# Kernel optimization log

Hardware: AMD Instinct MI355X
Metric: run time of the kernel (lower is better)

Reference implementation:

```python
import jax, jax.numpy as jnp
import numpy as np

HIDDEN = 2560
NUM_HEADS = 32
HEAD_DIM = HIDDEN // NUM_HEADS          # 80
ROTARY_DIM = int(0.4 * HEAD_DIM)        # 32 (partial rotary)
ROPE_BASE = 10000.0
SCALE = HEAD_DIM ** -0.5


def _apply_partial_rope(x, pos):
    # x: [B, S, H, D], pos: [B, S] int. NeoX-style rotation on first ROTARY_DIM dims.
    half = ROTARY_DIM // 2
    inv_freq = 1.0 / (ROPE_BASE ** (jnp.arange(half, dtype=jnp.float32) / half))
    ang = pos.astype(jnp.float32)[..., None] * inv_freq      # [B, S, half]
    cos = jnp.cos(ang)[:, :, None, :]                        # [B, S, 1, half]
    sin = jnp.sin(ang)[:, :, None, :]
    x1 = x[..., :half]
    x2 = x[..., half:ROTARY_DIM]
    x_pass = x[..., ROTARY_DIM:]
    o1 = x1 * cos - x2 * sin
    o2 = x2 * cos + x1 * sin
    return jnp.concatenate([o1, o2, x_pass], axis=-1)


def setup_inputs() -> dict:
    key = jax.random.key(0)
    ks = jax.random.split(key, 5)
    B, S = 2, 2048
    hidden_states = jax.random.normal(ks[0], (B, S, HIDDEN), dtype=jnp.float32)
    position_ids = jnp.tile(jnp.arange(S, dtype=jnp.int32)[None, :], (B, 1))
    w_std = HIDDEN ** -0.5
    Wqkv = jax.random.normal(ks[1], (HIDDEN, 3 * HIDDEN), dtype=jnp.float32) * w_std
    bqkv = jax.random.normal(ks[2], (3 * HIDDEN,), dtype=jnp.float32) * 0.02
    Wd = jax.random.normal(ks[3], (HIDDEN, HIDDEN), dtype=jnp.float32) * w_std
    bd = jax.random.normal(ks[4], (HIDDEN,), dtype=jnp.float32) * 0.02
    return {"position_ids": position_ids, "hidden_states": hidden_states,
            "Wqkv": Wqkv, "bqkv": bqkv, "Wd": Wd, "bd": bd}


def reference(position_ids, hidden_states, Wqkv, bqkv, Wd, bd):
    B, S, _ = hidden_states.shape
    qkv = hidden_states @ Wqkv + bqkv                         # [B, S, 3*HIDDEN]
    q, k, v = jnp.split(qkv, 3, axis=-1)
    q = q.reshape(B, S, NUM_HEADS, HEAD_DIM)
    k = k.reshape(B, S, NUM_HEADS, HEAD_DIM)
    v = v.reshape(B, S, NUM_HEADS, HEAD_DIM)
    q = _apply_partial_rope(q, position_ids)
    k = _apply_partial_rope(k, position_ids)
    # causal self-attention (RadixAttention prefill with empty prefix)
    scores = jnp.einsum('bqhd,bkhd->bhqk', q, k) * SCALE      # [B, H, S, S]
    causal = jnp.tril(jnp.ones((S, S), dtype=bool))
    scores = jnp.where(causal[None, None], scores, jnp.finfo(scores.dtype).min)
    probs = jax.nn.softmax(scores, axis=-1)
    attn = jnp.einsum('bhqk,bkhd->bqhd', probs, v).reshape(B, S, HIDDEN)
    return attn @ Wd + bd
```

## Files before the change

### kernel.cpp

```cpp
#include <hip/hip_runtime.h>

#define HIDDEN 2560
#define NHEADS 32
#define HDIM 80
#define DPAD 96
#define SEQ 2048
#define M_TOK 4096
#define N_QKV 7680
#define ATT_SCALE 0.11180339887498949f

typedef __attribute__((ext_vector_type(4))) float f32x4;
typedef __attribute__((ext_vector_type(16))) float f32x16;
typedef __attribute__((ext_vector_type(4))) int i32x4;
typedef __attribute__((ext_vector_type(8))) short bf16x8;
typedef __attribute__((ext_vector_type(8))) unsigned short ushort8;

#define BAR() asm volatile("s_barrier" ::: "memory")

__device__ __forceinline__ unsigned short f2bf(float f) {
    unsigned int u = __float_as_uint(f);
    u += 0x7FFFu + ((u >> 16) & 1u);
    return (unsigned short)(u >> 16);
}
__device__ __forceinline__ float bf2f(unsigned short h) {
    return __uint_as_float(((unsigned int)h) << 16);
}

__device__ __forceinline__ void async_copy16(unsigned short* lds, const unsigned short* g) {
    __builtin_amdgcn_global_load_lds((const __attribute__((address_space(1))) void*)g,
                                     (__attribute__((address_space(3))) void*)lds, 16, 0, 0);
}

__device__ __forceinline__ int cvt_pk_bf16(float lo, float hi) {
    int d;
    asm("v_cvt_pk_bf16_f32 %0, %1, %2" : "=v"(d) : "v"(lo), "v"(hi));
    return d;
}

__global__ __launch_bounds__(256) void cvt_kernel(const float* __restrict__ in,
                                                  unsigned short* __restrict__ out, int n8) {
    int i = blockIdx.x * 256 + threadIdx.x;
    if (i >= n8) return;
    const float4* p = (const float4*)in + (size_t)i * 2;
    float4 a = p[0], b = p[1];
    ushort8 o;
    o[0] = f2bf(a.x); o[1] = f2bf(a.y); o[2] = f2bf(a.z); o[3] = f2bf(a.w);
    o[4] = f2bf(b.x); o[5] = f2bf(b.y); o[6] = f2bf(b.z); o[7] = f2bf(b.w);
    *((ushort8*)out + i) = o;
}

__global__ __launch_bounds__(256) void transpose_kernel(const float* __restrict__ in,
                                                        unsigned short* __restrict__ out,
                                                        int R, int C) {
    __shared__ unsigned short tile[64][66];
    const int r0 = blockIdx.y * 64, c0 = blockIdx.x * 64;
    const int t = threadIdx.x;
#pragma unroll
    for (int rep = 0; rep < 16; ++rep) {
        int idx = rep * 256 + t;
        int i = idx >> 6, j = idx & 63;
        tile[i][j] = f2bf(in[(size_t)(r0 + i) * C + (c0 + j)]);
    }
    __syncthreads();
#pragma unroll
    for (int rep = 0; rep < 16; ++rep) {
        int idx = rep * 256 + t;
        int j = idx >> 6, i = idx & 63;
        out[(size_t)(c0 + j) * R + (r0 + i)] = tile[i][j];
    }
}

template <int OUT_BF16>
__global__ __launch_bounds__(512, 2) void gemm256(const unsigned short* __restrict__ A,
                                                  const unsigned short* __restrict__ Bt,
                                                  const float* __restrict__ bias,
                                                  void* __restrict__ C,
                                                  int M, int N, int K) {
    __shared__ __align__(16) unsigned short S[4][16384];
    const int t = threadIdx.x;
    const int lane = t & 63, wid = t >> 6;
    const int wm = wid >> 2, wn = wid & 3;
    const int l15 = lane & 15, lhi = lane >> 4;

    const int cpx = (int)gridDim.x >> 3;
    const int wg = ((int)blockIdx.x % 8) * cpx + ((int)blockIdx.x >> 3);
    const int bm = (wg & 15) * 256;
    const int bn = (wg >> 4) * 256;

    int srow[2], scol[2];
#pragma unroll
    for (int c = 0; c < 2; ++c) {
        int idx = t + c * 512;
        srow[c] = idx >> 2;
        scol[c] = ((idx & 3) ^ ((srow[c] >> 1) & 3)) * 8;
    }
    const unsigned short* Abase = A + (size_t)bm * K;
    const unsigned short* Bbase = Bt + (size_t)bn * K;
    const int NT = K >> 6;

    int aoff[8], boff[4];
#pragma unroll
    for (int i = 0; i < 8; ++i) {
        int r = wm * 128 + i * 16 + l15;
        aoff[i] = r * 32 + ((lhi ^ ((r >> 1) & 3)) * 8);
    }
#pragma unroll
    for (int f = 0; f < 4; ++f) {
        int r = wn * 64 + f * 16 + l15;
        boff[f] = 8192 + r * 32 + ((lhi ^ ((r >> 1) & 3)) * 8);
    }

    f32x4 acc[8][4] = {};

#define STAGE_A(J) { const int j_ = (J); unsigned short* d = &S[j_ & 3][0];            \
    _Pragma("unroll")                                                                  \
    for (int c = 0; c < 2; ++c)                                                        \
        async_copy16(d + (t + c * 512) * 8,                                            \
                     Abase + (size_t)srow[c] * K + j_ * 32 + scol[c]); }
#define STAGE_B(J) { const int j_ = (J); unsigned short* d = &S[j_ & 3][8192];         \
    _Pragma("unroll")                                                                  \
    for (int c = 0; c < 2; ++c)                                                        \
        async_copy16(d + (t + c * 512) * 8,                                            \
                     Bbase + (size_t)srow[c] * K + j_ * 32 + scol[c]); }

#define PERIOD(J, VM, DOSTAGE) {                                                       \
    const int jp_ = (J);                                                               \
    asm volatile("s_waitcnt vmcnt(" #VM ")" ::: "memory");                             \
    BAR();                                                                             \
    const unsigned short* sl = &S[jp_ & 3][0];                                         \
    if (DOSTAGE) STAGE_A(jp_ + 3);                                                     \
    bf16x8 bq[4], afr[4];                                                              \
    _Pragma("unroll")                                                                  \
    for (int f = 0; f < 4; ++f) bq[f] = *(const bf16x8*)(sl + boff[f]);                \
    _Pragma("unroll")                                                                  \
    for (int i = 0; i < 4; ++i) afr[i] = *(const bf16x8*)(sl + aoff[i]);               \
    __builtin_amdgcn_s_setprio(1);                                                     \
    _Pragma("unroll")                                                                  \
    for (int i = 0; i < 4; ++i)                                                        \
        _Pragma("unroll")                                                              \
        for (int f = 0; f < 4; ++f)                                                    \
            acc[i][f] = __builtin_amdgcn_mfma_f32_16x16x32_bf16(afr[i], bq[f],         \
                                                                acc[i][f], 0, 0, 0);   \
    __builtin_amdgcn_s_setprio(0);                                                     \
    if (DOSTAGE) STAGE_B(jp_ + 3);                                                     \
    _Pragma("unroll")                                                                  \
    for (int i = 0; i < 4; ++i) afr[i] = *(const bf16x8*)(sl + aoff[4 + i]);           \
    __builtin_amdgcn_s_setprio(1);                                                     \
    _Pragma("unroll")                                                                  \
    for (int i = 0; i < 4; ++i)                                                        \
        _Pragma("unroll")                                                              \
        for (int f = 0; f < 4; ++f)                                                    \
            acc[4 + i][f] = __builtin_amdgcn_mfma_f32_16x16x32_bf16(afr[i], bq[f],     \
                                                                    acc[4 + i][f],     \
                                                                    0, 0, 0);          \
    __builtin_amdgcn_s_setprio(0); }

    STAGE_A(0); STAGE_B(0);
    STAGE_A(1); STAGE_B(1);
    STAGE_A(2); STAGE_B(2);

    for (int T = 0; T < NT - 2; ++T) {
        PERIOD(2 * T, 8, 1);
        PERIOD(2 * T + 1, 8, 1);
    }
    PERIOD(2 * NT - 4, 8, 1);
    PERIOD(2 * NT - 3, 8, 0);
    PERIOD(2 * NT - 2, 4, 0);
    PERIOD(2 * NT - 1, 0, 0);

#undef PERIOD
#undef STAGE_A
#undef STAGE_B

#pragma unroll
    for (int f = 0; f < 4; ++f) {
        const int col = bn + wn * 64 + f * 16 + l15;
        const float bv = bias[col];
#pragma unroll
        for (int i = 0; i < 8; ++i) {
            const int row0 = bm + wm * 128 + i * 16 + lhi * 4;
#pragma unroll
            for (int r = 0; r < 4; ++r) {
                float v = acc[i][f][r] + bv;
                if (OUT_BF16)
                    ((unsigned short*)C)[(size_t)(row0 + r) * N + col] = f2bf(v);
                else
                    ((float*)C)[(size_t)(row0 + r) * N + col] = v;
            }
        }
    }
}

__global__ __launch_bounds__(256) void pack_rope_kernel(const unsigned short* __restrict__ qkv,
                                                        const int* __restrict__ pos_ids,
                                                        unsigned short* __restrict__ Qb,
                                                        unsigned short* __restrict__ Kb,
                                                        unsigned short* __restrict__ Vt) {
    int g = blockIdx.x * 256 + threadIdx.x;
    int s = g & (SEQ - 1);
    int bh = g >> 11;
    int b = bh >> 5;
    int h = bh & 31;
    int m = b * SEQ + s;
    const unsigned short* base = qkv + (size_t)m * N_QKV + h * HDIM;
    unsigned short* Qrow = Qb + ((size_t)bh * SEQ + s) * DPAD;
    unsigned short* Krow = Kb + ((size_t)bh * SEQ + s) * DPAD;
    unsigned short* Vcol = Vt + (size_t)bh * HDIM * SEQ + s;

    float pos = (float)pos_ids[m];
    float qv[32], kv[32];
#pragma unroll
    for (int c = 0; c < 4; ++c) {
        ushort8 qc = *(const ushort8*)(base + c * 8);
        ushort8 kc = *(const ushort8*)(base + HIDDEN + c * 8);
#pragma unroll
        for (int j = 0; j < 8; ++j) {
            qv[c * 8 + j] = bf2f(qc[j]);
            kv[c * 8 + j] = bf2f(kc[j]);
        }
    }
#pragma unroll
    for (int d = 0; d < 16; ++d) {
        float inv = __expf(-(float)d * 0.5756462732485115f);
        float ang = pos * inv;
        float sn, cs;
        __sincosf(ang, &sn, &cs);
        float qcs = cs * ATT_SCALE, qsn = sn * ATT_SCALE;
        float x1 = qv[d], x2 = qv[d + 16];
        qv[d] = x1 * qcs - x2 * qsn;
        qv[d + 16] = x2 * qcs + x1 * qsn;
        x1 = kv[d]; x2 = kv[d + 16];
        kv[d] = x1 * cs - x2 * sn;
        kv[d + 16] = x2 * cs + x1 * sn;
    }
#pragma unroll
    for (int c = 0; c < 4; ++c) {
        ushort8 qo, ko;
#pragma unroll
        for (int j = 0; j < 8; ++j) {
            qo[j] = f2bf(qv[c * 8 + j]);
            ko[j] = f2bf(kv[c * 8 + j]);
        }
        *(ushort8*)(Qrow + c * 8) = qo;
        *(ushort8*)(Krow + c * 8) = ko;
    }
#pragma unroll
    for (int c = 4; c < 10; ++c) {
        ushort8 qc = *(const ushort8*)(base + c * 8);
        ushort8 qo;
#pragma unroll
        for (int j = 0; j < 8; ++j) qo[j] = f2bf(bf2f(qc[j]) * ATT_SCALE);
        *(ushort8*)(Qrow + c * 8) = qo;
        *(ushort8*)(Krow + c * 8) = *(const ushort8*)(base + HIDDEN + c * 8);
    }
#pragma unroll
    for (int d = 0; d < HDIM; ++d) Vcol[(size_t)d * SEQ] = base[2 * HIDDEN + d];
}

__global__ __launch_bounds__(512) void flash_kernel(const unsigned short* __restrict__ Qb,
                                                    const unsigned short* __restrict__ Kb,
                                                    const unsigned short* __restrict__ Vt,
                                                    unsigned short* __restrict__ attn) {
    __shared__ __align__(16) unsigned short Klds[64 * 128];
    __shared__ __align__(16) unsigned short Vlds[96 * 64];

    const int bh = blockIdx.x;
    const int qb = 7 - (int)blockIdx.y;
    const int q0b = qb * 256;
    const int nkt = 4 * qb + 4;
    const int t = threadIdx.x;
    const int lane = t & 63, wid = t >> 6;
    const int l31 = lane & 31, h = lane >> 5, l7 = lane & 7;
    const int q0w = q0b + wid * 32;
    const int swz = l7 << 3;

    const unsigned short* Kbase = Kb + (size_t)bh * SEQ * DPAD;
    const unsigned short* Vbase = Vt + (size_t)bh * HDIM * SEQ;

    bf16x8 qf[5];
    {
        const unsigned short* Qrow = Qb + ((size_t)bh * SEQ + q0w + l31) * DPAD + h * 8;
#pragma unroll
        for (int dc = 0; dc < 5; ++dc) qf[dc] = *(const bf16x8*)(Qrow + dc * 16);
    }

    ((int*)Vlds)[2560 + t] = 0;

    f32x16 acc0 = {}, acc1 = {}, acc2 = {};
    float mrow = -1e30f, lrow = 0.f;

    const int kidx1 = 512 + t;
    const int kr0 = t / 10, kc0 = t % 10;
    const int kr1 = kidx1 / 10, kc1 = kidx1 % 10;
    const int vr0 = t >> 3, vc0 = t & 7;
    const int vr1 = (512 + t) >> 3, vc1 = t & 7;
    const int kd0 = kr0 * 128 + ((kc0 * 8) ^ ((kr0 & 7) << 3));
    const int kd1 = kr1 * 128 + ((kc1 * 8) ^ ((kr1 & 7) << 3));
    const int vd0 = vr0 * 64 + ((vc0 * 8) ^ ((vr0 & 7) << 3));
    const int vd1 = vr1 * 64 + ((vc1 * 8) ^ ((vr1 & 7) << 3));

    ushort8 kreg0, kreg1, vreg0, vreg1;
    kreg0 = *(const ushort8*)(Kbase + (size_t)kr0 * DPAD + kc0 * 8);
    if (t < 128) kreg1 = *(const ushort8*)(Kbase + (size_t)kr1 * DPAD + kc1 * 8);
    vreg0 = *(const ushort8*)(Vbase + (size_t)vr0 * SEQ + vc0 * 8);
    if (t < 128) vreg1 = *(const ushort8*)(Vbase + (size_t)vr1 * SEQ + vc1 * 8);

    for (int kt = 0; kt < nkt; ++kt) {
        const int k0 = kt * 64;
        __syncthreads();
        *(ushort8*)(Klds + kd0) = kreg0;
        if (t < 128) *(ushort8*)(Klds + kd1) = kreg1;
        *(ushort8*)(Vlds + vd0) = vreg0;
        if (t < 128) *(ushort8*)(Vlds + vd1) = vreg1;
        __syncthreads();
        if (kt + 1 < nkt) {
            const int kn = k0 + 64;
            kreg0 = *(const ushort8*)(Kbase + (size_t)(kn + kr0) * DPAD + kc0 * 8);
            if (t < 128) kreg1 = *(const ushort8*)(Kbase + (size_t)(kn + kr1) * DPAD + kc1 * 8);
            vreg0 = *(const ushort8*)(Vbase + (size_t)vr0 * SEQ + kn + vc0 * 8);
            if (t < 128) vreg1 = *(const ushort8*)(Vbase + (size_t)vr1 * SEQ + kn + vc1 * 8);
        }
        if (k0 > q0w + 31) continue;

        f32x16 s0 = {}, s1 = {};
        __builtin_amdgcn_s_setprio(1);
#pragma unroll
        for (int dc = 0; dc < 5; ++dc) {
            const int co = (dc * 16 + h * 8) ^ swz;
            bf16x8 ka = *(const bf16x8*)(Klds + l31 * 128 + co);
            bf16x8 kb2 = *(const bf16x8*)(Klds + (32 + l31) * 128 + co);
            s0 = __builtin_amdgcn_mfma_f32_32x32x16_bf16(ka, qf[dc], s0, 0, 0, 0);
            s1 = __builtin_amdgcn_mfma_f32_32x32x16_bf16(kb2, qf[dc], s1, 0, 0, 0);
        }
        __builtin_amdgcn_s_setprio(0);

        const int qg = q0w + l31;
        if (k0 + 63 > q0w) {
#pragma unroll
            for (int r = 0; r < 16; ++r) {
                const int kg = k0 + (r & 3) + 8 * (r >> 2) + 4 * h;
                if (kg > qg) s0[r] = -2e30f;
                if (kg + 32 > qg) s1[r] = -2e30f;
            }
        }
        float pmax = s0[0];
#pragma unroll
        for (int r = 1; r < 16; ++r) pmax = fmaxf(pmax, s0[r]);
#pragma unroll
        for (int r = 0; r < 16; ++r) pmax = fmaxf(pmax, s1[r]);
        pmax = fmaxf(pmax, __shfl_xor(pmax, 32, 64));
        if (!__all(pmax <= mrow + 8.0f)) {
            float mnew = fmaxf(mrow, pmax);
            float scl = __expf(mrow - mnew);
            mrow = mnew;
            lrow *= scl;
#pragma unroll
            for (int r = 0; r < 16; ++r) {
                float sq = __shfl(scl, (r & 3) + 8 * (r >> 2) + 4 * h, 64);
                acc0[r] *= sq; acc1[r] *= sq; acc2[r] *= sq;
            }
        }
        float ps = 0.f;
#pragma unroll
        for (int r = 0; r < 16; ++r) { s0[r] = __expf(s0[r] - mrow); ps += s0[r]; }
#pragma unroll
        for (int r = 0; r < 16; ++r) { s1[r] = __expf(s1[r] - mrow); ps += s1[r]; }
        lrow += ps + __shfl_xor(ps, 32, 64);
        i32x4 af[2][2];
#pragma unroll
        for (int ks = 0; ks < 2; ++ks) {
            const f32x16& sv = ks ? s1 : s0;
            int pk0[2], pk1[2], pk2[2], pk3[2];
#pragma unroll
            for (int i = 0; i < 2; ++i) {
                pk0[i] = cvt_pk_bf16(sv[2 * i], sv[2 * i + 1]);
                pk1[i] = cvt_pk_bf16(sv[4 + 2 * i], sv[5 + 2 * i]);
                pk2[i] = cvt_pk_bf16(sv[8 + 2 * i], sv[9 + 2 * i]);
                pk3[i] = cvt_pk_bf16(sv[12 + 2 * i], sv[13 + 2 * i]);
            }
#pragma unroll
            for (int i = 0; i < 2; ++i) {
                const int o0 = __shfl_xor(pk0[i], 32, 64);
                const int o1 = __shfl_xor(pk1[i], 32, 64);
                af[ks][0][i]     = h ? o1     : pk0[i];
                af[ks][0][2 + i] = h ? pk1[i] : o0;
                const int o2 = __shfl_xor(pk2[i], 32, 64);
                const int o3 = __shfl_xor(pk3[i], 32, 64);
                af[ks][1][i]     = h ? o3     : pk2[i];
                af[ks][1][2 + i] = h ? pk3[i] : o2;
            }
        }
        __builtin_amdgcn_s_setprio(1);
#pragma unroll
        for (int ds = 0; ds < 3; ++ds) {
            f32x16& ac = ds == 0 ? acc0 : (ds == 1 ? acc1 : acc2);
            const int vrow = (ds * 32 + l31) * 64;
#pragma unroll
            for (int ks = 0; ks < 2; ++ks)
#pragma unroll
                for (int kh = 0; kh < 2; ++kh) {
                    bf16x8 vb = *(const bf16x8*)(Vlds + vrow + ((ks * 32 + kh * 16 + h * 8) ^ swz));
                    bf16x8 pa = __builtin_bit_cast(bf16x8, af[ks][kh]);
                    ac = __builtin_amdgcn_mfma_f32_32x32x16_bf16(pa, vb, ac, 0, 0, 0);
                }
        }
        __builtin_amdgcn_s_setprio(0);
    }

    const int hh = bh & 31, b = bh >> 5;
    const float linv = 1.0f / lrow;
#pragma unroll
    for (int r = 0; r < 16; ++r) {
        const int ql = (r & 3) + 8 * (r >> 2) + 4 * h;
        const float lv = __shfl(linv, ql, 64);
        const int row = b * SEQ + q0b + wid * 32 + ql;
        unsigned short* orow = attn + (size_t)row * HIDDEN + hh * HDIM;
        orow[l31] = f2bf(acc0[r] * lv);
        orow[32 + l31] = f2bf(acc1[r] * lv);
        if (l31 < 16) orow[64 + l31] = f2bf(acc2[r] * lv);
    }
}

extern "C" void kernel_launch(void* const* d_in, const int* in_sizes, int n_in,
                              void* d_out, int out_size, void* d_ws, size_t ws_size,
                              hipStream_t stream) {
    const int* pos = (const int*)d_in[0];
    const float* hid = (const float*)d_in[1];
    const float* Wqkv = (const float*)d_in[2];
    const float* bqkv = (const float*)d_in[3];
    const float* Wd = (const float*)d_in[4];
    const float* bd = (const float*)d_in[5];
    float* out = (float*)d_out;
    char* ws = (char*)d_ws;

    unsigned short* WqkvT = (unsigned short*)(ws);
    unsigned short* WdT   = (unsigned short*)(ws + 39321600);
    unsigned short* Xbf   = (unsigned short*)(ws + 52428800);
    unsigned short* qkv   = (unsigned short*)(ws + 73400320);
    unsigned short* Qbuf  = (unsigned short*)(ws + 136314880);
    unsigned short* Kbuf  = (unsigned short*)(ws + 161480704);
    unsigned short* Vt    = (unsigned short*)(ws + 186646528);
    unsigned short* attnb = Xbf;

    cvt_kernel<<<(M_TOK * HIDDEN / 8 + 255) / 256, 256, 0, stream>>>(hid, Xbf, M_TOK * HIDDEN / 8);
    transpose_kernel<<<dim3(N_QKV / 64, HIDDEN / 64), 256, 0, stream>>>(Wqkv, WqkvT, HIDDEN, N_QKV);
    transpose_kernel<<<dim3(HIDDEN / 64, HIDDEN / 64), 256, 0, stream>>>(Wd, WdT, HIDDEN, HIDDEN);
    gemm256<1><<<(M_TOK / 256) * (N_QKV / 256), 512, 0, stream>>>(Xbf, WqkvT, bqkv, qkv,
                                                                  M_TOK, N_QKV, HIDDEN);
    pack_rope_kernel<<<(64 * SEQ) / 256, 256, 0, stream>>>(qkv, pos, Qbuf, Kbuf, Vt);
    flash_kernel<<<dim3(64, 8), 512, 0, stream>>>(Qbuf, Kbuf, Vt, attnb);
    gemm256<0><<<(M_TOK / 256) * (HIDDEN / 256), 512, 0, stream>>>(attnb, WdT, bd, out,
                                                                   M_TOK, HIDDEN, HIDDEN);
}
```

Measured before the change: 387.8 us.

## Switch GEMM to double-buffered 64-wide K tiles with wider swizzle

```diff
diff --git a/kernel.cpp b/kernel.cpp
--- a/kernel.cpp
+++ b/kernel.cpp
@@ -76,7 +76,7 @@
                                                   const float* __restrict__ bias,
                                                   void* __restrict__ C,
                                                   int M, int N, int K) {
-    __shared__ __align__(16) unsigned short S[4][16384];
+    __shared__ __align__(16) unsigned short S[2][32768];
     const int t = threadIdx.x;
     const int lane = t & 63, wid = t >> 6;
     const int wm = wid >> 2, wn = wid & 3;
@@ -87,12 +87,12 @@
     const int bm = (wg & 15) * 256;
     const int bn = (wg >> 4) * 256;
 
-    int srow[2], scol[2];
-#pragma unroll
-    for (int c = 0; c < 2; ++c) {
+    int srow[4], scol[4];
+#pragma unroll
+    for (int c = 0; c < 4; ++c) {
         int idx = t + c * 512;
-        srow[c] = idx >> 2;
-        scol[c] = ((idx & 3) ^ ((srow[c] >> 1) & 3)) * 8;
+        srow[c] = idx >> 3;
+        scol[c] = ((idx & 7) ^ (srow[c] & 7)) * 8;
     }
     const unsigned short* Abase = A + (size_t)bm * K;
     const unsigned short* Bbase = Bt + (size_t)bn * K;
@@ -102,73 +102,75 @@
 #pragma unroll
     for (int i = 0; i < 8; ++i) {
         int r = wm * 128 + i * 16 + l15;
-        aoff[i] = r * 32 + ((lhi ^ ((r >> 1) & 3)) * 8);
+        aoff[i] = r * 64 + ((lhi ^ (r & 7)) * 8);
     }
 #pragma unroll
     for (int f = 0; f < 4; ++f) {
         int r = wn * 64 + f * 16 + l15;
-        boff[f] = 8192 + r * 32 + ((lhi ^ ((r >> 1) & 3)) * 8);
+        boff[f] = 16384 + r * 64 + ((lhi ^ (r & 7)) * 8);
     }
 
     f32x4 acc[8][4] = {};
 
-#define STAGE_A(J) { const int j_ = (J); unsigned short* d = &S[j_ & 3][0];            \
+#define STAGE_A(T1) { unsigned short* d = &S[(T1) & 1][0];                             \
     _Pragma("unroll")                                                                  \
-    for (int c = 0; c < 2; ++c)                                                        \
+    for (int c = 0; c < 4; ++c)                                                        \
         async_copy16(d + (t + c * 512) * 8,                                            \
-                     Abase + (size_t)srow[c] * K + j_ * 32 + scol[c]); }
-#define STAGE_B(J) { const int j_ = (J); unsigned short* d = &S[j_ & 3][8192];         \
+                     Abase + (size_t)srow[c] * K + (T1) * 64 + scol[c]); }
+#define STAGE_B(T1) { unsigned short* d = &S[(T1) & 1][16384];                         \
     _Pragma("unroll")                                                                  \
-    for (int c = 0; c < 2; ++c)                                                        \
+    for (int c = 0; c < 4; ++c)                                                        \
         async_copy16(d + (t + c * 512) * 8,                                            \
-                     Bbase + (size_t)srow[c] * K + j_ * 32 + scol[c]); }
-
-#define PERIOD(J, VM, DOSTAGE) {                                                       \
-    const int jp_ = (J);                                                               \
-    asm volatile("s_waitcnt vmcnt(" #VM ")" ::: "memory");                             \
-    BAR();                                                                             \
-    const unsigned short* sl = &S[jp_ & 3][0];                                         \
-    if (DOSTAGE) STAGE_A(jp_ + 3);                                                     \
-    bf16x8 bq[4], afr[4];                                                              \
-    _Pragma("unroll")                                                                  \
-    for (int f = 0; f < 4; ++f) bq[f] = *(const bf16x8*)(sl + boff[f]);                \
-    _Pragma("unroll")                                                                  \
-    for (int i = 0; i < 4; ++i) afr[i] = *(const bf16x8*)(sl + aoff[i]);               \
-    __builtin_amdgcn_s_setprio(1);                                                     \
-    _Pragma("unroll")                                                                  \
-    for (int i = 0; i < 4; ++i)                                                        \
-        _Pragma("unroll")                                                              \
-        for (int f = 0; f < 4; ++f)                                                    \
-            acc[i][f] = __builtin_amdgcn_mfma_f32_16x16x32_bf16(afr[i], bq[f],         \
-                                                                acc[i][f], 0, 0, 0);   \
-    __builtin_amdgcn_s_setprio(0);                                                     \
-    if (DOSTAGE) STAGE_B(jp_ + 3);                                                     \
-    _Pragma("unroll")                                                                  \
-    for (int i = 0; i < 4; ++i) afr[i] = *(const bf16x8*)(sl + aoff[4 + i]);           \
-    __builtin_amdgcn_s_setprio(1);                                                     \
-    _Pragma("unroll")                                                                  \
-    for (int i = 0; i < 4; ++i)                                                        \
-        _Pragma("unroll")                                                              \
-        for (int f = 0; f < 4; ++f)                                                    \
-            acc[4 + i][f] = __builtin_amdgcn_mfma_f32_16x16x32_bf16(afr[i], bq[f],     \
-                                                                    acc[4 + i][f],     \
-                                                                    0, 0, 0);          \
-    __builtin_amdgcn_s_setprio(0); }
+                     Bbase + (size_t)srow[c] * K + (T1) * 64 + scol[c]); }
 
     STAGE_A(0); STAGE_B(0);
-    STAGE_A(1); STAGE_B(1);
-    STAGE_A(2); STAGE_B(2);
-
-    for (int T = 0; T < NT - 2; ++T) {
-        PERIOD(2 * T, 8, 1);
-        PERIOD(2 * T + 1, 8, 1);
-    }
-    PERIOD(2 * NT - 4, 8, 1);
-    PERIOD(2 * NT - 3, 8, 0);
-    PERIOD(2 * NT - 2, 4, 0);
-    PERIOD(2 * NT - 1, 0, 0);
-
-#undef PERIOD
+
+    for (int T = 0; T < NT; ++T) {
+        asm volatile("s_waitcnt vmcnt(0)" ::: "memory");
+        BAR();
+        const unsigned short* sl = &S[T & 1][0];
+        bf16x8 bq[4][2], afr[4][2];
+#pragma unroll
+        for (int f = 0; f < 4; ++f)
+#pragma unroll
+            for (int kk = 0; kk < 2; ++kk)
+                bq[f][kk] = *(const bf16x8*)(sl + (boff[f] ^ (kk * 32)));
+#pragma unroll
+        for (int i = 0; i < 4; ++i)
+#pragma unroll
+            for (int kk = 0; kk < 2; ++kk)
+                afr[i][kk] = *(const bf16x8*)(sl + (aoff[i] ^ (kk * 32)));
+        if (T + 1 < NT) STAGE_A(T + 1);
+        BAR();
+        __builtin_amdgcn_s_setprio(1);
+#pragma unroll
+        for (int i = 0; i < 4; ++i)
+#pragma unroll
+            for (int f = 0; f < 4; ++f)
+#pragma unroll
+                for (int kk = 0; kk < 2; ++kk)
+                    acc[i][f] = __builtin_amdgcn_mfma_f32_16x16x32_bf16(afr[i][kk], bq[f][kk],
+                                                                        acc[i][f], 0, 0, 0);
+        __builtin_amdgcn_s_setprio(0);
+        bf16x8 af2[4][2];
+#pragma unroll
+        for (int i = 0; i < 4; ++i)
+#pragma unroll
+            for (int kk = 0; kk < 2; ++kk)
+                af2[i][kk] = *(const bf16x8*)(sl + (aoff[4 + i] ^ (kk * 32)));
+        if (T + 1 < NT) STAGE_B(T + 1);
+        __builtin_amdgcn_s_setprio(1);
+#pragma unroll
+        for (int i = 0; i < 4; ++i)
+#pragma unroll
+            for (int f = 0; f < 4; ++f)
+#pragma unroll
+                for (int kk = 0; kk < 2; ++kk)
+                    acc[4 + i][f] = __builtin_amdgcn_mfma_f32_16x16x32_bf16(af2[i][kk], bq[f][kk],
+                                                                            acc[4 + i][f], 0, 0, 0);
+        __builtin_amdgcn_s_setprio(0);
+    }
+
 #undef STAGE_A
 #undef STAGE_B
 
```

Result: slower. 397.3 us (+2.5%).

## Split GEMM tile work across 16 waves with 1024-thread blocks

Applied to the files above, without the earlier changes.

```diff
diff --git a/kernel.cpp b/kernel.cpp
--- a/kernel.cpp
+++ b/kernel.cpp
@@ -71,11 +71,11 @@
 }
 
 template <int OUT_BF16>
-__global__ __launch_bounds__(512, 2) void gemm256(const unsigned short* __restrict__ A,
-                                                  const unsigned short* __restrict__ Bt,
-                                                  const float* __restrict__ bias,
-                                                  void* __restrict__ C,
-                                                  int M, int N, int K) {
+__global__ __launch_bounds__(1024, 4) void gemm256(const unsigned short* __restrict__ A,
+                                                   const unsigned short* __restrict__ Bt,
+                                                   const float* __restrict__ bias,
+                                                   void* __restrict__ C,
+                                                   int M, int N, int K) {
     __shared__ __align__(16) unsigned short S[4][16384];
     const int t = threadIdx.x;
     const int lane = t & 63, wid = t >> 6;
@@ -87,21 +87,16 @@
     const int bm = (wg & 15) * 256;
     const int bn = (wg >> 4) * 256;
 
-    int srow[2], scol[2];
-#pragma unroll
-    for (int c = 0; c < 2; ++c) {
-        int idx = t + c * 512;
-        srow[c] = idx >> 2;
-        scol[c] = ((idx & 3) ^ ((srow[c] >> 1) & 3)) * 8;
-    }
+    const int srow = t >> 2;
+    const int scol = ((t & 3) ^ ((srow >> 1) & 3)) * 8;
     const unsigned short* Abase = A + (size_t)bm * K;
     const unsigned short* Bbase = Bt + (size_t)bn * K;
-    const int NT = K >> 6;
-
-    int aoff[8], boff[4];
-#pragma unroll
-    for (int i = 0; i < 8; ++i) {
-        int r = wm * 128 + i * 16 + l15;
+    const int NP = K >> 5;
+
+    int aoff[4], boff[4];
+#pragma unroll
+    for (int i = 0; i < 4; ++i) {
+        int r = wm * 64 + i * 16 + l15;
         aoff[i] = r * 32 + ((lhi ^ ((r >> 1) & 3)) * 8);
     }
 #pragma unroll
@@ -110,18 +105,14 @@
         boff[f] = 8192 + r * 32 + ((lhi ^ ((r >> 1) & 3)) * 8);
     }
 
-    f32x4 acc[8][4] = {};
-
-#define STAGE_A(J) { const int j_ = (J); unsigned short* d = &S[j_ & 3][0];            \
-    _Pragma("unroll")                                                                  \
-    for (int c = 0; c < 2; ++c)                                                        \
-        async_copy16(d + (t + c * 512) * 8,                                            \
-                     Abase + (size_t)srow[c] * K + j_ * 32 + scol[c]); }
-#define STAGE_B(J) { const int j_ = (J); unsigned short* d = &S[j_ & 3][8192];         \
-    _Pragma("unroll")                                                                  \
-    for (int c = 0; c < 2; ++c)                                                        \
-        async_copy16(d + (t + c * 512) * 8,                                            \
-                     Bbase + (size_t)srow[c] * K + j_ * 32 + scol[c]); }
+    f32x4 acc[4][4] = {};
+
+#define STAGE_A(J) { const int j_ = (J);                                               \
+    async_copy16(&S[j_ & 3][0] + t * 8,                                                \
+                 Abase + (size_t)srow * K + j_ * 32 + scol); }
+#define STAGE_B(J) { const int j_ = (J);                                               \
+    async_copy16(&S[j_ & 3][8192] + t * 8,                                             \
+                 Bbase + (size_t)srow * K + j_ * 32 + scol); }
 
 #define PERIOD(J, VM, DOSTAGE) {                                                       \
     const int jp_ = (J);                                                               \
@@ -129,29 +120,29 @@
     BAR();                                                                             \
     const unsigned short* sl = &S[jp_ & 3][0];                                         \
     if (DOSTAGE) STAGE_A(jp_ + 3);                                                     \
-    bf16x8 bq[4], afr[4];                                                              \
+    bf16x8 bq[4], afr[2];                                                              \
     _Pragma("unroll")                                                                  \
     for (int f = 0; f < 4; ++f) bq[f] = *(const bf16x8*)(sl + boff[f]);                \
-    _Pragma("unroll")                                                                  \
-    for (int i = 0; i < 4; ++i) afr[i] = *(const bf16x8*)(sl + aoff[i]);               \
+    afr[0] = *(const bf16x8*)(sl + aoff[0]);                                           \
+    afr[1] = *(const bf16x8*)(sl + aoff[1]);                                           \
     __builtin_amdgcn_s_setprio(1);                                                     \
     _Pragma("unroll")                                                                  \
-    for (int i = 0; i < 4; ++i)                                                        \
+    for (int i = 0; i < 2; ++i)                                                        \
         _Pragma("unroll")                                                              \
         for (int f = 0; f < 4; ++f)                                                    \
             acc[i][f] = __builtin_amdgcn_mfma_f32_16x16x32_bf16(afr[i], bq[f],         \
                                                                 acc[i][f], 0, 0, 0);   \
     __builtin_amdgcn_s_setprio(0);                                                     \
     if (DOSTAGE) STAGE_B(jp_ + 3);                                                     \
-    _Pragma("unroll")                                                                  \
-    for (int i = 0; i < 4; ++i) afr[i] = *(const bf16x8*)(sl + aoff[4 + i]);           \
+    afr[0] = *(const bf16x8*)(sl + aoff[2]);                                           \
+    afr[1] = *(const bf16x8*)(sl + aoff[3]);                                           \
     __builtin_amdgcn_s_setprio(1);                                                     \
     _Pragma("unroll")                                                                  \
-    for (int i = 0; i < 4; ++i)                                                        \
+    for (int i = 0; i < 2; ++i)                                                        \
         _Pragma("unroll")                                                              \
         for (int f = 0; f < 4; ++f)                                                    \
-            acc[4 + i][f] = __builtin_amdgcn_mfma_f32_16x16x32_bf16(afr[i], bq[f],     \
-                                                                    acc[4 + i][f],     \
+            acc[2 + i][f] = __builtin_amdgcn_mfma_f32_16x16x32_bf16(afr[i], bq[f],     \
+                                                                    acc[2 + i][f],     \
                                                                     0, 0, 0);          \
     __builtin_amdgcn_s_setprio(0); }
 
@@ -159,14 +150,12 @@
     STAGE_A(1); STAGE_B(1);
     STAGE_A(2); STAGE_B(2);
 
-    for (int T = 0; T < NT - 2; ++T) {
-        PERIOD(2 * T, 8, 1);
-        PERIOD(2 * T + 1, 8, 1);
-    }
-    PERIOD(2 * NT - 4, 8, 1);
-    PERIOD(2 * NT - 3, 8, 0);
-    PERIOD(2 * NT - 2, 4, 0);
-    PERIOD(2 * NT - 1, 0, 0);
+    for (int p = 0; p < NP - 3; ++p) {
+        PERIOD(p, 4, 1);
+    }
+    PERIOD(NP - 3, 4, 0);
+    PERIOD(NP - 2, 2, 0);
+    PERIOD(NP - 1, 0, 0);
 
 #undef PERIOD
 #undef STAGE_A
@@ -177,8 +166,8 @@
         const int col = bn + wn * 64 + f * 16 + l15;
         const float bv = bias[col];
 #pragma unroll
-        for (int i = 0; i < 8; ++i) {
-            const int row0 = bm + wm * 128 + i * 16 + lhi * 4;
+        for (int i = 0; i < 4; ++i) {
+            const int row0 = bm + wm * 64 + i * 16 + lhi * 4;
 #pragma unroll
             for (int r = 0; r < 4; ++r) {
                 float v = acc[i][f][r] + bv;
@@ -445,10 +434,10 @@
     cvt_kernel<<<(M_TOK * HIDDEN / 8 + 255) / 256, 256, 0, stream>>>(hid, Xbf, M_TOK * HIDDEN / 8);
     transpose_kernel<<<dim3(N_QKV / 64, HIDDEN / 64), 256, 0, stream>>>(Wqkv, WqkvT, HIDDEN, N_QKV);
     transpose_kernel<<<dim3(HIDDEN / 64, HIDDEN / 64), 256, 0, stream>>>(Wd, WdT, HIDDEN, HIDDEN);
-    gemm256<1><<<(M_TOK / 256) * (N_QKV / 256), 512, 0, stream>>>(Xbf, WqkvT, bqkv, qkv,
-                                                                  M_TOK, N_QKV, HIDDEN);
+    gemm256<1><<<(M_TOK / 256) * (N_QKV / 256), 1024, 0, stream>>>(Xbf, WqkvT, bqkv, qkv,
+                                                                   M_TOK, N_QKV, HIDDEN);
     pack_rope_kernel<<<(64 * SEQ) / 256, 256, 0, stream>>>(qkv, pos, Qbuf, Kbuf, Vt);
     flash_kernel<<<dim3(64, 8), 512, 0, stream>>>(Qbuf, Kbuf, Vt, attnb);
-    gemm256<0><<<(M_TOK / 256) * (HIDDEN / 256), 512, 0, stream>>>(attnb, WdT, bd, out,
-                                                                   M_TOK, HIDDEN, HIDDEN);
-}
+    gemm256<0><<<(M_TOK / 256) * (HIDDEN / 256), 1024, 0, stream>>>(attnb, WdT, bd, out,
+                                                                    M_TOK, HIDDEN, HIDDEN);
+}
```

Result: no change. 380.4 us, median of 2 (-1.9%).
